# Performance work log

Hardware: AMD Instinct MI355X
Metric: run time of the kernel (lower is better)

Reference implementation:

```python
import jax, jax.numpy as jnp
import numpy as np

DIM = 3          # algebra dimension (3D Clifford algebra Cl(3,0))
NB = 2 ** DIM    # 8 blades
C_IN, C_OUT = 4, 4
K = 3            # conv kernel size
S = 48           # spatial size (== mask_size)
B = 4            # batch size
HID = 128


def _build_algebra():
    """Cayley table of Cl(3,0) with blades ordered by (grade, bitmask), and the
    path matrix M[p, bj, bk] = sum_bi cayley[bi,bj,bk] restricted to grade-triple p."""
    n = NB
    blades = sorted(range(n), key=lambda b: (bin(b).count('1'), b))
    idx = {b: i for i, b in enumerate(blades)}
    grades = np.array([bin(b).count('1') for b in blades])
    cay = np.zeros((n, n, n), dtype=np.float32)
    for a in range(n):
        for b in range(n):
            s = 1
            t = a >> 1
            while t:
                s *= (-1) ** bin(t & b).count('1')
                t >>= 1
            cay[idx[a], idx[b], idx[a ^ b]] = s  # Euclidean metric: no extra signs
    ng = DIM + 1
    path_id = -np.ones((ng, ng, ng), dtype=int)
    p = 0
    for gi in range(ng):
        for gj in range(ng):
            for gk in range(ng):
                if np.any(cay[np.ix_(np.where(grades == gi)[0], np.where(grades == gj)[0], np.where(grades == gk)[0])] != 0):
                    path_id[gi, gj, gk] = p
                    p += 1
    P = p  # == product_paths_sum == 20 for Cl(3,0)
    M = np.zeros((P, n, n), dtype=np.float32)
    for i in range(n):
        for j in range(n):
            for k in range(n):
                c = cay[i, j, k]
                if c != 0.0:
                    M[path_id[grades[i], grades[j], grades[k]], j, k] += c
    return M, P

CAYLEY_M, P = _build_algebra()


def _circular_mask(ks):
    c = (ks - 1) / 2.0
    zz, yy, xx = np.ogrid[:ks, :ks, :ks]
    d = np.sqrt((xx - c) ** 2 + (yy - c) ** 2 + (zz - c) ** 2)
    return (d <= c).astype(np.float32)


def _rel_pos_mv():
    """Kernel-grid offsets embedded as grade-1 multivectors: (K^3, NB)."""
    ax = np.linspace(-1.0, 1.0, K).astype(np.float32)
    gx, gy, gz = np.meshgrid(ax, ax, ax, indexing='ij')
    pos = np.stack([gx, gy, gz], -1).reshape(-1, DIM)
    mv = np.zeros((K ** DIM, NB), dtype=np.float32)
    mv[:, 1:1 + DIM] = pos  # grade-1 blade slots are indices 1..3
    return mv


def setup_inputs() -> dict:
    key = jax.random.key(0)
    ks = jax.random.split(key, 4)
    x = jax.random.normal(ks[0], (B, C_IN, S, S, S, NB), jnp.float32)
    w0 = jax.random.normal(ks[1], (2 * NB, HID), jnp.float32) / np.sqrt(2 * NB)
    w1 = jax.random.normal(ks[2], (HID, HID), jnp.float32) / np.sqrt(HID)
    w2 = jax.random.normal(ks[3], (HID, C_OUT * C_IN * P), jnp.float32) / np.sqrt(HID)
    return {
        'x': x,
        'w0': w0, 'b0': jnp.zeros((HID,), jnp.float32),
        'w1': w1, 'b1': jnp.zeros((HID,), jnp.float32),
        'w2': w2, 'b2': jnp.zeros((C_OUT * C_IN * P,), jnp.float32),
        'bias_param': jnp.zeros((C_OUT, 1, 1, 1, 1), jnp.float32),
    }


def reference(x, w0, b0, w1, b1, w2, b2, bias_param):
    # 1) masked global pooling -> per-sample per-blade condition (B, NB)
    mask = jnp.asarray(_circular_mask(S))
    cond = jnp.einsum('bcxyzn,xyz->bn', x, mask) / (mask.sum() * C_IN)

    # 2) per-sample dynamic kernel generation (vmapped kernel network)
    rel = jnp.asarray(_rel_pos_mv())               # (X, NB), X = K^3
    X = K ** DIM
    feat = jnp.concatenate([
        jnp.broadcast_to(rel[None], (B, X, NB)),
        jnp.broadcast_to(cond[:, None, :], (B, X, NB)),
    ], axis=-1)                                     # (B, X, 2*NB)
    h = jax.nn.gelu(feat @ w0 + b0)
    h = jax.nn.gelu(h @ w1 + b1)
    w = (h @ w2 + b2).reshape(B, X, C_OUT, C_IN, P)  # per-path geometric-product weights

    # 3) assemble blade-level kernel via sparse Cayley contraction
    M = jnp.asarray(CAYLEY_M)                       # (P, NB_in_blade, NB_out_blade)
    ker = jnp.einsum('bxoip,pjk->bokijx', w, M)     # (B, o, bk, i, bj, X)
    kernels = ker.reshape(B * C_OUT * NB, C_IN * NB, K, K, K)

    # 4) grouped conv: one kernel bank per sample (feature_group_count = B)
    inp = jnp.transpose(x, (0, 1, 5, 2, 3, 4)).reshape(1, B * C_IN * NB, S, S, S)
    out = jax.lax.conv_general_dilated(
        inp, kernels, window_strides=(1, 1, 1), padding='SAME',
        dimension_numbers=('NCDHW', 'OIDHW', 'NCDHW'), feature_group_count=B)
    out = out.reshape(B, C_OUT, NB, S, S, S)
    out = jnp.transpose(out, (0, 1, 3, 4, 5, 2))    # (B, c_out, S,S,S, NB)

    # 5) multivector bias embedded at blade dims (0,)
    bias = jnp.zeros((C_OUT, 1, 1, 1, NB), x.dtype).at[..., 0:1].set(bias_param)
    return out + bias
```

## Files before the change

### kernel.cpp

```cpp
#include <hip/hip_runtime.h>
#include <cmath>

#define SS 48
#define S3 110592
#define NB 8
#define CIN 4
#define COUT 4
#define HID 128
#define XT 27
#define NP 20
#define BATCH 4
#define PD 50
#define PD2 2500
#define PD3 125000
#define SLABV 648
#define SLABS 5184
#define WGRP 3072

typedef __attribute__((ext_vector_type(8))) short short8;
typedef __attribute__((ext_vector_type(4))) float f32x4;

struct Tables {
    int   pid[64];
    float sgn[64];
};

__device__ __forceinline__ unsigned short bf16_rne(float f) {
    union { float f; unsigned u; } c; c.f = f;
    unsigned r = c.u + 0x7FFF + ((c.u >> 16) & 1);
    return (unsigned short)(r >> 16);
}

__device__ __forceinline__ float gelu_tanh(float v) {
    const float c = 0.7978845608028654f;
    float u = c * (v + 0.044715f * v * v * v);
    return 0.5f * v * (1.0f + tanhf(u));
}

__global__ __launch_bounds__(256)
void pack_cond_kernel(const float* __restrict__ x, unsigned short* __restrict__ xb,
                      float* __restrict__ partial) {
    int b  = blockIdx.y;
    int pv = blockIdx.x * 256 + threadIdx.x;
    __shared__ float sacc[8];
    if (threadIdx.x < 8) sacc[threadIdx.x] = 0.0f;
    __syncthreads();
    float acc[8];
#pragma unroll
    for (int n = 0; n < 8; ++n) acc[n] = 0.0f;
    if (pv < PD3) {
        int zp = pv / PD2, rem = pv % PD2, yp = rem / PD, xp = rem % PD;
        int z = zp - 1, y = yp - 1, xx = xp - 1;
        unsigned short ob[32];
        bool interior = (unsigned)z < 48u && (unsigned)y < 48u && (unsigned)xx < 48u;
        if (interior) {
            int v = (z * 48 + y) * 48 + xx;
            float vals[32];
#pragma unroll
            for (int i = 0; i < 4; ++i) {
                const f32x4* p = (const f32x4*)(x + (((size_t)(b * 4 + i)) * S3 + v) * 8);
                f32x4 a = p[0], c4 = p[1];
                vals[i * 8 + 0] = a[0];  vals[i * 8 + 1] = a[1];
                vals[i * 8 + 2] = a[2];  vals[i * 8 + 3] = a[3];
                vals[i * 8 + 4] = c4[0]; vals[i * 8 + 5] = c4[1];
                vals[i * 8 + 6] = c4[2]; vals[i * 8 + 7] = c4[3];
            }
            int dx = 2 * xx - 47, dy = 2 * y - 47, dz = 2 * z - 47;
            if (dx * dx + dy * dy + dz * dz <= 2209) {
#pragma unroll
                for (int n = 0; n < 8; ++n)
                    acc[n] = vals[n] + vals[8 + n] + vals[16 + n] + vals[24 + n];
            }
#pragma unroll
            for (int k = 0; k < 32; ++k) ob[k] = bf16_rne(vals[k]);
        } else {
#pragma unroll
            for (int k = 0; k < 32; ++k) ob[k] = 0;
        }
        short8* dst = (short8*)(xb + ((size_t)b * PD3 + pv) * 32);
#pragma unroll
        for (int q = 0; q < 4; ++q) {
            short8 s;
#pragma unroll
            for (int e = 0; e < 8; ++e) s[e] = (short)ob[q * 8 + e];
            dst[q] = s;
        }
    }
#pragma unroll
    for (int n = 0; n < 8; ++n) {
        float a = acc[n];
        for (int off = 32; off; off >>= 1) a += __shfl_down(a, off);
        if ((threadIdx.x & 63) == 0) atomicAdd(&sacc[n], a);
    }
    __syncthreads();
    if (threadIdx.x < 8)
        partial[((size_t)b * 512 + blockIdx.x) * 8 + threadIdx.x] = sacc[threadIdx.x];
}

__global__ __launch_bounds__(256)
void cond_reduce(const float* __restrict__ partial, float* __restrict__ cond) {
    int b = blockIdx.x, t = threadIdx.x;
    __shared__ float red[32][8];
    int ch = t & 7, seg = t >> 3;
    float s = 0.0f;
    for (int j = seg; j < 489; j += 32)
        s += partial[((size_t)b * 512 + j) * 8 + ch];
    red[seg][ch] = s;
    __syncthreads();
    if (t < 8) {
        float s2 = 0.0f;
#pragma unroll
        for (int q = 0; q < 32; ++q) s2 += red[q][t];
        cond[b * 8 + t] = s2;
    }
}

__global__ __launch_bounds__(128)
void mlp12(const float* __restrict__ cond,
           const float* __restrict__ w0, const float* __restrict__ b0,
           const float* __restrict__ w1, const float* __restrict__ b1,
           float* __restrict__ h2out, float inv_norm) {
    int bx = blockIdx.x;
    int b = bx / XT, tap = bx % XT;
    int t = threadIdx.x;
    __shared__ float feat[16];
    __shared__ float h1[HID];
    if (t < 16) {
        float v = 0.0f;
        if (t < 8) {
            if (t == 1) v = (float)(tap / 9) - 1.0f;
            else if (t == 2) v = (float)((tap / 3) % 3) - 1.0f;
            else if (t == 3) v = (float)(tap % 3) - 1.0f;
        } else {
            v = cond[b * 8 + (t - 8)] * inv_norm;
        }
        feat[t] = v;
    }
    __syncthreads();
    float s = b0[t];
#pragma unroll
    for (int k = 0; k < 16; ++k) s += feat[k] * w0[k * HID + t];
    h1[t] = gelu_tanh(s);
    __syncthreads();
    float a0 = b1[t], a1 = 0.0f, a2 = 0.0f, a3 = 0.0f;
#pragma unroll
    for (int k = 0; k < HID; k += 4) {
        a0 += h1[k + 0] * w1[(k + 0) * HID + t];
        a1 += h1[k + 1] * w1[(k + 1) * HID + t];
        a2 += h1[k + 2] * w1[(k + 2) * HID + t];
        a3 += h1[k + 3] * w1[(k + 3) * HID + t];
    }
    h2out[(size_t)bx * HID + t] = gelu_tanh((a0 + a1) + (a2 + a3));
}

__global__ __launch_bounds__(320)
void mlp3(const float* __restrict__ h2in, const float* __restrict__ w2,
          const float* __restrict__ b2, unsigned short* __restrict__ wb, Tables tb) {
    int bx = blockIdx.x;
    int b = bx / XT, tap = bx % XT;
    int t = threadIdx.x;
    __shared__ float h2[HID];
    __shared__ float wrow[320];
    if (t < HID) h2[t] = h2in[(size_t)bx * HID + t];
    __syncthreads();
    float a0 = b2[t], a1 = 0.0f, a2 = 0.0f, a3 = 0.0f;
#pragma unroll
    for (int k = 0; k < HID; k += 4) {
        a0 += h2[k + 0] * w2[(size_t)(k + 0) * 320 + t];
        a1 += h2[k + 1] * w2[(size_t)(k + 1) * 320 + t];
        a2 += h2[k + 2] * w2[(size_t)(k + 2) * 320 + t];
        a3 += h2[k + 3] * w2[(size_t)(k + 3) * 320 + t];
    }
    wrow[t] = (a0 + a1) + (a2 + a3);
    __syncthreads();
    if (t < 128) {
        int m = t >> 2, cq = t & 3;
        int o = m >> 3, bk = m & 7;
        short8 sv;
#pragma unroll
        for (int e = 0; e < 8; ++e) {
            int c = cq * 8 + e;
            int i = c >> 3, bj = c & 7, jk = bj * 8 + bk;
            sv[e] = (short)bf16_rne(tb.sgn[jk] * wrow[o * 80 + i * 20 + tb.pid[jk]]);
        }
        int g  = (tap / 9) * 3 + (tap % 3);
        int ky = (tap % 9) / 3;
        int half = m >> 4, mm = m & 15;
        size_t tile = (size_t)(b * 27 + g * 3 + ky) * 1024;
        *(short8*)(wb + tile + half * 512 + (mm + cq * 16) * 8) = sv;
    }
}

__global__ __launch_bounds__(256, 3)
void conv_lds(const unsigned short* __restrict__ xb, const unsigned short* __restrict__ wb,
              const float* __restrict__ bias, float* __restrict__ out) {
    __shared__ __align__(16) short lds[4 * SLABS];
    __shared__ __align__(16) short wlds[2][WGRP];
    int b  = blockIdx.y;
    int bx = blockIdx.x;
    int tx = bx % 3, ty = (bx / 3) % 12, tz = bx / 36;
    int X0 = tx * 16, Y0 = ty * 4, Z0 = tz * 4;
    int tid = threadIdx.x, lane = tid & 63, wave = tid >> 6;

    const unsigned short* xsrc = xb + (size_t)b * PD3 * 32 +
        ((size_t)Z0 * PD2 + (size_t)Y0 * PD + X0) * 32 + wave * 8;
#pragma unroll
    for (int k = 0; k < 11; ++k) {
        int h0 = k * 64, h = h0 + lane;
        if (h < SLABV) {
            int hz = h / 108, rem = h % 108, hy = rem / 18, hx = rem % 18;
            __builtin_amdgcn_global_load_lds(
                (const unsigned int*)(xsrc + ((size_t)hz * PD2 + hy * PD + hx) * 32),
                (unsigned int*)&lds[wave * SLABS + h0 * 8], 16, 0, 0);
        }
    }
    const unsigned short* wsrc = wb + (size_t)b * 27648;
#pragma unroll
    for (int k = 0; k < 2; ++k) {
        int c = tid + k * 256;
        if (c < 384)
            __builtin_amdgcn_global_load_lds((const unsigned int*)(wsrc + c * 8),
                (unsigned int*)&wlds[0][(c & ~63) * 8], 16, 0, 0);
    }
    __syncthreads();

    int col = lane & 15, kl = lane >> 4;
    const short* lbase = &lds[kl * SLABS + (wave * 108 + col) * 8];

    f32x4 acc[2][4];
#pragma unroll
    for (int mh = 0; mh < 2; ++mh)
#pragma unroll
        for (int r = 0; r < 4; ++r)
#pragma unroll
            for (int e = 0; e < 4; ++e) acc[mh][r][e] = 0.0f;

#pragma unroll
    for (int g = 0; g < 9; ++g) {
        const int kz = g / 3, kx = g % 3;
        const int cur = g & 1;
        if (g < 8) {
            const unsigned short* wsrc2 = wsrc + (size_t)(g + 1) * WGRP;
#pragma unroll
            for (int k = 0; k < 2; ++k) {
                int c = tid + k * 256;
                if (c < 384)
                    __builtin_amdgcn_global_load_lds((const unsigned int*)(wsrc2 + c * 8),
                        (unsigned int*)&wlds[cur ^ 1][(c & ~63) * 8], 16, 0, 0);
            }
        }
        const short* wgrp = &wlds[cur][lane * 8];
        short8 bfv[6];
#pragma unroll
        for (int u = 0; u < 6; ++u)
            bfv[u] = *(const short8*)(lbase + (kz * 108 + u * 18 + kx) * 8);
#pragma unroll
        for (int ky = 0; ky < 3; ++ky) {
            short8 a0 = *(const short8*)(wgrp + ky * 1024);
            short8 a1 = *(const short8*)(wgrp + ky * 1024 + 512);
#pragma unroll
            for (int r = 0; r < 4; ++r) {
                acc[0][r] = __builtin_amdgcn_mfma_f32_16x16x32_bf16(a0, bfv[r + ky], acc[0][r], 0, 0, 0);
                acc[1][r] = __builtin_amdgcn_mfma_f32_16x16x32_bf16(a1, bfv[r + ky], acc[1][r], 0, 0, 0);
            }
        }
        if (g < 8) __syncthreads();
    }

    int xc = X0 + col;
    int z  = Z0 + wave;
#pragma unroll
    for (int mh = 0; mh < 2; ++mh) {
        int m0 = kl * 4 + mh * 16;
        int o = m0 >> 3, bk0 = m0 & 7;
        float bi = (bk0 == 0) ? bias[o] : 0.0f;
#pragma unroll
        for (int r = 0; r < 4; ++r) {
            int y = Y0 + r;
            int vox = (z * 48 + y) * 48 + xc;
            f32x4 v = acc[mh][r];
            v[0] += bi;
            *(f32x4*)(out + (((size_t)(b * 4 + o)) * S3 + vox) * 8 + bk0) = v;
        }
    }
}

static inline int pc_host(int v) { return __builtin_popcount(v); }

extern "C" void kernel_launch(void* const* d_in, const int* in_sizes, int n_in,
                              void* d_out, int out_size, void* d_ws, size_t ws_size,
                              hipStream_t stream) {
    const float* x    = (const float*)d_in[0];
    const float* w0   = (const float*)d_in[1];
    const float* b0   = (const float*)d_in[2];
    const float* w1   = (const float*)d_in[3];
    const float* b1   = (const float*)d_in[4];
    const float* w2   = (const float*)d_in[5];
    const float* b2   = (const float*)d_in[6];
    const float* bias = (const float*)d_in[7];
    float* out = (float*)d_out;

    float* ws      = (float*)d_ws;
    float* partial = ws;
    float* cond    = ws + 16384;
    float* h2buf   = ws + 16448;
    unsigned short* wbb = (unsigned short*)(ws + 30272);
    unsigned short* xb  = wbb + 110592;

    int cnt = 0;
    for (int z = 0; z < SS; ++z) {
        int dz = 2 * z - 47;
        for (int y = 0; y < SS; ++y) {
            int dy = 2 * y - 47;
            for (int xx = 0; xx < SS; ++xx) {
                int dx = 2 * xx - 47;
                if (dx * dx + dy * dy + dz * dz <= 2209) ++cnt;
            }
        }
    }
    float inv_norm = 1.0f / ((float)cnt * (float)CIN);

    int pidtab[4][4][4];
    {
        bool ex[4][4][4] = {};
        for (int A = 0; A < 8; ++A)
            for (int B = 0; B < 8; ++B)
                ex[pc_host(A)][pc_host(B)][pc_host(A ^ B)] = true;
        int p = 0;
        for (int gi = 0; gi < 4; ++gi)
            for (int gj = 0; gj < 4; ++gj)
                for (int gk = 0; gk < 4; ++gk)
                    pidtab[gi][gj][gk] = ex[gi][gj][gk] ? p++ : -1;
    }
    static const int blades[8] = {0, 1, 2, 4, 3, 5, 6, 7};
    Tables tb;
    for (int bj = 0; bj < 8; ++bj) {
        for (int bk = 0; bk < 8; ++bk) {
            int bmj = blades[bj], bmk = blades[bk];
            int bma = bmj ^ bmk;
            int sgn = 1, t = bma >> 1;
            while (t) {
                if (pc_host(t & bmj) & 1) sgn = -sgn;
                t >>= 1;
            }
            tb.sgn[bj * 8 + bk] = (float)sgn;
            tb.pid[bj * 8 + bk] = pidtab[pc_host(bma)][pc_host(bmj)][pc_host(bmk)];
        }
    }

    pack_cond_kernel<<<dim3(489, BATCH), dim3(256), 0, stream>>>(x, xb, partial);
    cond_reduce<<<dim3(BATCH), dim3(256), 0, stream>>>(partial, cond);
    mlp12<<<dim3(BATCH * XT), dim3(128), 0, stream>>>(cond, w0, b0, w1, b1, h2buf, inv_norm);
    mlp3<<<dim3(BATCH * XT), dim3(320), 0, stream>>>(h2buf, w2, b2, wbb, tb);
    conv_lds<<<dim3(432, BATCH), dim3(256), 0, stream>>>(xb, wbb, bias, out);
}
```

Baseline: 71.20 us.

## Hold conv weights in registers and split waves by output half instead of z

```diff
diff --git a/kernel.cpp b/kernel.cpp
--- a/kernel.cpp
+++ b/kernel.cpp
@@ -15,7 +15,6 @@
 #define PD3 125000
 #define SLABV 648
 #define SLABS 5184
-#define WGRP 3072
 
 typedef __attribute__((ext_vector_type(8))) short short8;
 typedef __attribute__((ext_vector_type(4))) float f32x4;
@@ -195,7 +194,6 @@
 void conv_lds(const unsigned short* __restrict__ xb, const unsigned short* __restrict__ wb,
               const float* __restrict__ bias, float* __restrict__ out) {
     __shared__ __align__(16) short lds[4 * SLABS];
-    __shared__ __align__(16) short wlds[2][WGRP];
     int b  = blockIdx.y;
     int bx = blockIdx.x;
     int tx = bx % 3, ty = (bx / 3) % 12, tz = bx / 36;
@@ -214,71 +212,68 @@
                 (unsigned int*)&lds[wave * SLABS + h0 * 8], 16, 0, 0);
         }
     }
-    const unsigned short* wsrc = wb + (size_t)b * 27648;
-#pragma unroll
-    for (int k = 0; k < 2; ++k) {
-        int c = tid + k * 256;
-        if (c < 384)
-            __builtin_amdgcn_global_load_lds((const unsigned int*)(wsrc + c * 8),
-                (unsigned int*)&wlds[0][(c & ~63) * 8], 16, 0, 0);
-    }
-    __syncthreads();
 
     int col = lane & 15, kl = lane >> 4;
-    const short* lbase = &lds[kl * SLABS + (wave * 108 + col) * 8];
+    int mh = wave >> 1, zp = (wave & 1) * 2;
+
+    const unsigned short* wgl = wb + (size_t)b * 27648 + mh * 512 + lane * 8;
+    short8 wcur[9], wnxt[9];
+#pragma unroll
+    for (int t9 = 0; t9 < 9; ++t9)
+        wcur[t9] = *(const short8*)(wgl + (size_t)t9 * 1024);
+    __syncthreads();
 
     f32x4 acc[2][4];
 #pragma unroll
-    for (int mh = 0; mh < 2; ++mh)
+    for (int s = 0; s < 2; ++s)
 #pragma unroll
         for (int r = 0; r < 4; ++r)
 #pragma unroll
-            for (int e = 0; e < 4; ++e) acc[mh][r][e] = 0.0f;
-
-#pragma unroll
-    for (int g = 0; g < 9; ++g) {
-        const int kz = g / 3, kx = g % 3;
-        const int cur = g & 1;
-        if (g < 8) {
-            const unsigned short* wsrc2 = wsrc + (size_t)(g + 1) * WGRP;
-#pragma unroll
-            for (int k = 0; k < 2; ++k) {
-                int c = tid + k * 256;
-                if (c < 384)
-                    __builtin_amdgcn_global_load_lds((const unsigned int*)(wsrc2 + c * 8),
-                        (unsigned int*)&wlds[cur ^ 1][(c & ~63) * 8], 16, 0, 0);
-            }
-        }
-        const short* wgrp = &wlds[cur][lane * 8];
-        short8 bfv[6];
-#pragma unroll
-        for (int u = 0; u < 6; ++u)
-            bfv[u] = *(const short8*)(lbase + (kz * 108 + u * 18 + kx) * 8);
-#pragma unroll
-        for (int ky = 0; ky < 3; ++ky) {
-            short8 a0 = *(const short8*)(wgrp + ky * 1024);
-            short8 a1 = *(const short8*)(wgrp + ky * 1024 + 512);
-#pragma unroll
-            for (int r = 0; r < 4; ++r) {
-                acc[0][r] = __builtin_amdgcn_mfma_f32_16x16x32_bf16(a0, bfv[r + ky], acc[0][r], 0, 0, 0);
-                acc[1][r] = __builtin_amdgcn_mfma_f32_16x16x32_bf16(a1, bfv[r + ky], acc[1][r], 0, 0, 0);
-            }
-        }
-        if (g < 8) __syncthreads();
+            for (int e = 0; e < 4; ++e) acc[s][r][e] = 0.0f;
+
+#pragma unroll
+    for (int kz = 0; kz < 3; ++kz) {
+        if (kz < 2) {
+#pragma unroll
+            for (int t9 = 0; t9 < 9; ++t9)
+                wnxt[t9] = *(const short8*)(wgl + (size_t)((kz + 1) * 9 + t9) * 1024);
+        }
+#pragma unroll
+        for (int kx = 0; kx < 3; ++kx) {
+#pragma unroll
+            for (int s = 0; s < 2; ++s) {
+                const short* lb = &lds[kl * SLABS + ((zp + s + kz) * 108 + col + kx) * 8];
+                short8 bfv[6];
+#pragma unroll
+                for (int u = 0; u < 6; ++u)
+                    bfv[u] = *(const short8*)(lb + u * 144);
+#pragma unroll
+                for (int ky = 0; ky < 3; ++ky) {
+                    short8 a = wcur[kx * 3 + ky];
+#pragma unroll
+                    for (int r = 0; r < 4; ++r)
+                        acc[s][r] = __builtin_amdgcn_mfma_f32_16x16x32_bf16(a, bfv[r + ky], acc[s][r], 0, 0, 0);
+                }
+            }
+        }
+        if (kz < 2) {
+#pragma unroll
+            for (int t9 = 0; t9 < 9; ++t9) wcur[t9] = wnxt[t9];
+        }
     }
 
     int xc = X0 + col;
-    int z  = Z0 + wave;
-#pragma unroll
-    for (int mh = 0; mh < 2; ++mh) {
-        int m0 = kl * 4 + mh * 16;
-        int o = m0 >> 3, bk0 = m0 & 7;
-        float bi = (bk0 == 0) ? bias[o] : 0.0f;
+    int m0 = kl * 4 + mh * 16;
+    int o = m0 >> 3, bk0 = m0 & 7;
+    float bi = (bk0 == 0) ? bias[o] : 0.0f;
+#pragma unroll
+    for (int s = 0; s < 2; ++s) {
+        int z = Z0 + zp + s;
 #pragma unroll
         for (int r = 0; r < 4; ++r) {
             int y = Y0 + r;
             int vox = (z * 48 + y) * 48 + xc;
-            f32x4 v = acc[mh][r];
+            f32x4 v = acc[s][r];
             v[0] += bi;
             *(f32x4*)(out + (((size_t)(b * 4 + o)) * S3 + vox) * 8 + bk0) = v;
         }
```

Result: faster. 69.29 us (-2.7%).
